# Optimization experiments

Measured on AMD Instinct MI355X. Metric: run time of the kernel, lower is better.

## Reference

```python
import jax, jax.numpy as jnp
import numpy as np

NUM_EXPERTS = 16
TOP_K = 2
INTER = 448  # per-expert intermediate dim


def setup_inputs() -> dict:
    key = jax.random.key(0)
    k1, k2, k3, k4, k5 = jax.random.split(key, 5)
    B, S, H = 4, 2048, 4096
    scale = 0.02
    return {
        "hid": jax.random.normal(k1, (B, S, H), dtype=jnp.float32),
        "gate_w": jax.random.normal(k2, (NUM_EXPERTS, H), dtype=jnp.float32) * scale,
        "u": jax.random.normal(k3, (NUM_EXPERTS * INTER, H), dtype=jnp.float32) * scale,
        "g": jax.random.normal(k4, (NUM_EXPERTS * INTER, H), dtype=jnp.float32) * scale,
        "d": jax.random.normal(k5, (H, NUM_EXPERTS * INTER), dtype=jnp.float32) * scale,
    }


def reference(hid, gate_w, u, g, d):
    B, S, H = hid.shape
    x = hid.reshape(-1, H)  # [bs, H], bs = B*S tokens
    bs = x.shape[0]

    # --- router: softmax over experts, top-k, renormalize, scatter to dense weights ---
    logits = x @ gate_w.T  # [bs, E]
    probs = jax.nn.softmax(logits.astype(jnp.float32), axis=-1)
    vals, idx = jax.lax.top_k(probs, TOP_K)  # [bs, k]
    vals = vals / jnp.sum(vals, axis=-1, keepdims=True)
    rows = jnp.arange(bs)[:, None]
    w = jnp.zeros((bs, NUM_EXPERTS), dtype=jnp.float32).at[rows, idx].set(vals)
    w = w.astype(x.dtype)  # sparse routing weights (zeros off the top-k)

    # --- experts: merged SwiGLU MLP, per-expert 448-wide slices of u/g/d ---
    gate_out = (x @ g.T).reshape(bs, NUM_EXPERTS, INTER)  # [bs, E, I]
    up_out = (x @ u.T).reshape(bs, NUM_EXPERTS, INTER)
    h = jax.nn.silu(gate_out) * up_out  # ir in the original code

    # down proj per expert, weighted by routing weights, summed over experts
    d_r = d.reshape(H, NUM_EXPERTS, INTER)
    out = jnp.einsum("bei,hei,be->bh", h, d_r, w)
    return out.reshape(B, S, H)
```

## Files before the change

### kernel.cpp

```cpp
#include <hip/hip_runtime.h>
#include <hip/hip_bf16.h>
#include <stdint.h>


#define NE    16
#define INTER 448
#define HDIM  4096
#define BS    8192
#define ROWS  (BS * 2)
#define NGU   896
#define CAP   8192

typedef __attribute__((ext_vector_type(8))) _Float16 half8;
typedef __attribute__((ext_vector_type(4))) _Float16 half4;
typedef __attribute__((ext_vector_type(4))) float    f32x4;

__device__ __forceinline__ void gld16(const _Float16* g, _Float16* l) {
    __builtin_amdgcn_global_load_lds(
        (const __attribute__((address_space(1))) void*)g,
        (__attribute__((address_space(3))) void*)l, 16, 0, 0);
}


__global__ __launch_bounds__(256) void k_convert_gu(const float* __restrict__ src,
                                                    _Float16* __restrict__ dst,
                                                    int col_off) {
    int64_t id  = (int64_t)blockIdx.x * 256 + threadIdx.x;
    int64_t k   = (id & 511) * 8;
    int64_t row = id >> 9;
    int     e   = (int)(row / 448);
    int64_t drow = (int64_t)e * NGU + col_off + (row - (int64_t)e * 448);
    const float4* s = reinterpret_cast<const float4*>(src + row * HDIM + k);
    float4 a = s[0], b = s[1];
    half8 o;
    o[0] = (_Float16)a.x; o[1] = (_Float16)a.y; o[2] = (_Float16)a.z; o[3] = (_Float16)a.w;
    o[4] = (_Float16)b.x; o[5] = (_Float16)b.y; o[6] = (_Float16)b.z; o[7] = (_Float16)b.w;
    *reinterpret_cast<half8*>(dst + drow * HDIM + k) = o;
}

__global__ __launch_bounds__(256) void k_convert_flat(const float* __restrict__ src,
                                                      _Float16* __restrict__ dst) {
    int64_t id = ((int64_t)blockIdx.x * 256 + threadIdx.x) * 8;
    const float4* s = reinterpret_cast<const float4*>(src + id);
    float4 a = s[0], b = s[1];
    half8 o;
    o[0] = (_Float16)a.x; o[1] = (_Float16)a.y; o[2] = (_Float16)a.z; o[3] = (_Float16)a.w;
    o[4] = (_Float16)b.x; o[5] = (_Float16)b.y; o[6] = (_Float16)b.z; o[7] = (_Float16)b.w;
    *reinterpret_cast<half8*>(dst + id) = o;
}

__global__ __launch_bounds__(64) void k_router(const float* __restrict__ x,
                                               const float* __restrict__ gw,
                                               _Float16* __restrict__ xh,
                                               int* __restrict__ counts,
                                               int* __restrict__ perm,
                                               float* __restrict__ rw) {
    int t = blockIdx.x;
    int lane = threadIdx.x;
    const float* xr = x + (int64_t)t * HDIM;
    double acc[NE];
#pragma unroll
    for (int e = 0; e < NE; e++) acc[e] = 0.0;
    for (int h = lane * 4; h < HDIM; h += 256) {
        float4 xv = *reinterpret_cast<const float4*>(xr + h);
        half4 o;
        o[0] = (_Float16)xv.x; o[1] = (_Float16)xv.y;
        o[2] = (_Float16)xv.z; o[3] = (_Float16)xv.w;
        *reinterpret_cast<half4*>(xh + (int64_t)t * HDIM + h) = o;
#pragma unroll
        for (int e = 0; e < NE; e++) {
            float4 gv = *reinterpret_cast<const float4*>(gw + e * HDIM + h);
            acc[e] += (double)xv.x * gv.x + (double)xv.y * gv.y
                    + (double)xv.z * gv.z + (double)xv.w * gv.w;
        }
    }
#pragma unroll
    for (int e = 0; e < NE; e++) {
#pragma unroll
        for (int off = 32; off > 0; off >>= 1)
            acc[e] += __shfl_xor(acc[e], off, 64);
    }
    if (lane == 0) {
        int i0 = 0; double l0 = acc[0];
        for (int e = 1; e < NE; e++) if (acc[e] > l0) { l0 = acc[e]; i0 = e; }
        double l1 = -1e300; int i1 = 0;
        for (int e = 0; e < NE; e++) if (e != i0 && acc[e] > l1) { l1 = acc[e]; i1 = e; }
        float w0 = 1.0f / (1.0f + __expf((float)(l1 - l0)));
        float w1 = 1.0f - w0;
        int p0 = atomicAdd(&counts[i0], 1);
        int p1 = atomicAdd(&counts[i1], 1);
        perm[i0 * CAP + p0] = t * 2;
        perm[i1 * CAP + p1] = t * 2 + 1;
        rw[t * 2]     = w0;
        rw[t * 2 + 1] = w1;
    }
}

template <int KTOT, bool DOWN>
__global__ __launch_bounds__(256, 3) void k_gemm(const _Float16* __restrict__ A,
                                                 const _Float16* __restrict__ B,
                                                 const int* __restrict__ counts,
                                                 const int* __restrict__ perm,
                                                 _Float16* __restrict__ gu_out,
                                                 float* __restrict__ out) {
    int e  = blockIdx.z;
    int nt = blockIdx.x;
    int cnt = counts[e];
    __shared__ __align__(16) _Float16 As[128 * 32];
    __shared__ __align__(16) _Float16 Bs[128 * 32];
    __shared__ int perm_s[128];
    int tid  = threadIdx.x;
    int lane = tid & 63, wave = tid >> 6;
    int wm = wave >> 1, wn = wave & 1;
    int lm = lane & 15, lq = lane >> 4;

    int rrow = lane >> 2;
    int cseg = (lane & 3) * 8;
    int row0 = wave * 16 + rrow;
    int row1 = 64 + wave * 16 + rrow;
    _Float16* As0 = &As[(wave * 16) * 32];
    _Float16* As1 = &As[(64 + wave * 16) * 32];
    _Float16* Bs0 = &Bs[(wave * 16) * 32];
    _Float16* Bs1 = &Bs[(64 + wave * 16) * 32];

    const _Float16 *b0, *b1;
    if (DOWN) {
        b0 = B + (int64_t)(nt * 128 + row0) * (NE * INTER) + e * INTER + cseg;
        b1 = B + (int64_t)(nt * 128 + row1) * (NE * INTER) + e * INTER + cseg;
    } else {
        b0 = B + ((int64_t)e * NGU + nt * 128 + row0) * HDIM + cseg;
        b1 = B + ((int64_t)e * NGU + nt * 128 + row1) * HDIM + cseg;
    }

    for (int mt = blockIdx.y; mt * 128 < cnt; mt += gridDim.y) {
        __syncthreads();
        if (tid < 128) {
            int r = mt * 128 + tid;
            perm_s[tid] = (r < cnt) ? perm[e * CAP + r] : -1;
        }
        __syncthreads();
        int pr0 = perm_s[row0], pr1 = perm_s[row1];
        const _Float16 *a0, *a1;
        if (DOWN) {
            a0 = A + (pr0 < 0 ? 0 : (int64_t)pr0 * INTER) + cseg;
            a1 = A + (pr1 < 0 ? 0 : (int64_t)pr1 * INTER) + cseg;
        } else {
            a0 = A + (pr0 < 0 ? 0 : (int64_t)(pr0 >> 1) * HDIM) + cseg;
            a1 = A + (pr1 < 0 ? 0 : (int64_t)(pr1 >> 1) * HDIM) + cseg;
        }
        const _Float16 *bb0 = b0, *bb1 = b1;

        f32x4 acc[4][4];
#pragma unroll
        for (int i = 0; i < 4; i++)
#pragma unroll
            for (int j = 0; j < 4; j++) acc[i][j] = (f32x4){0.f, 0.f, 0.f, 0.f};

#pragma unroll 1
        for (int kt = 0; kt < KTOT; kt += 32) {
            gld16(a0,  As0);  gld16(a1,  As1);
            gld16(bb0, Bs0);  gld16(bb1, Bs1);
            a0 += 32; a1 += 32; bb0 += 32; bb1 += 32;
            __syncthreads();
            half8 af[4], bfr[4];
#pragma unroll
            for (int mi = 0; mi < 4; mi++)
                af[mi] = *reinterpret_cast<const half8*>(&As[(wm * 64 + mi * 16 + lm) * 32 + lq * 8]);
#pragma unroll
            for (int ni = 0; ni < 4; ni++)
                bfr[ni] = *reinterpret_cast<const half8*>(&Bs[(wn * 64 + ni * 16 + lm) * 32 + lq * 8]);
#pragma unroll
            for (int mi = 0; mi < 4; mi++)
#pragma unroll
                for (int ni = 0; ni < 4; ni++)
                    acc[mi][ni] = __builtin_amdgcn_mfma_f32_16x16x32_f16(af[mi], bfr[ni], acc[mi][ni], 0, 0, 0);
            __syncthreads();
        }
#pragma unroll
        for (int mi = 0; mi < 4; mi++) {
#pragma unroll
            for (int r = 0; r < 4; r++) {
                int row = wm * 64 + mi * 16 + lq * 4 + r;
                int g = perm_s[row];
                if (g < 0) continue;
#pragma unroll
                for (int ni = 0; ni < 4; ni++) {
                    int col = nt * 128 + wn * 64 + ni * 16 + lm;
                    float v = acc[mi][ni][r];
                    if (DOWN) atomicAdd(&out[(int64_t)(g >> 1) * HDIM + col], v);
                    else      gu_out[(int64_t)g * NGU + col] = (_Float16)v;
                }
            }
        }
    }
}

__global__ __launch_bounds__(256) void k_swiglu(const _Float16* __restrict__ gu,
                                                const float* __restrict__ rw,
                                                _Float16* __restrict__ h) {
    int64_t id  = (int64_t)blockIdx.x * 256 + threadIdx.x;
    int64_t row = id / 56;
    int64_t j   = (id - row * 56) * 8;
    float w = rw[row];
    half8 gv = *reinterpret_cast<const half8*>(gu + row * NGU + j);
    half8 uv = *reinterpret_cast<const half8*>(gu + row * NGU + 448 + j);
    half8 o;
#pragma unroll
    for (int i = 0; i < 8; i++) {
        float g = (float)gv[i];
        float u = (float)uv[i];
        float s = g / (1.0f + __expf(-g));
        o[i] = (_Float16)(s * u * w);
    }
    *reinterpret_cast<half8*>(h + row * INTER + j) = o;
}

extern "C" void kernel_launch(void* const* d_in, const int* in_sizes, int n_in,
                              void* d_out, int out_size, void* d_ws, size_t ws_size,
                              hipStream_t stream) {
    (void)in_sizes; (void)n_in; (void)ws_size;
    const float* hid    = (const float*)d_in[0];
    const float* gate_w = (const float*)d_in[1];
    const float* u      = (const float*)d_in[2];
    const float* g      = (const float*)d_in[3];
    const float* d      = (const float*)d_in[4];
    float* out = (float*)d_out;

    char* w = (char*)d_ws;
    _Float16* xh    = (_Float16*)(w);
    _Float16* wgu   = (_Float16*)(w + 67108864);
    _Float16* d16   = (_Float16*)(w + 184549376);
    _Float16* gu    = (_Float16*)(w + 243269632);
    _Float16* hbuf  = (_Float16*)(w + 272629760);
    int*      perm  = (int*)     (w + 287309824);
    float*    rw    = (float*)   (w + 287834112);
    int*      cnts  = (int*)     (w + 287899648);

    hipMemsetAsync(d_out, 0, (size_t)out_size * sizeof(float), stream);
    hipMemsetAsync(cnts, 0, 64, stream);

    k_convert_gu<<<14336, 256, 0, stream>>>(g, wgu, 0);
    k_convert_gu<<<14336, 256, 0, stream>>>(u, wgu, 448);
    k_convert_flat<<<14336, 256, 0, stream>>>(d, d16);
    k_router<<<BS, 64, 0, stream>>>(hid, gate_w, xh, cnts, perm, rw);
    k_gemm<HDIM, false><<<dim3(7, 16, NE), 256, 0, stream>>>(xh, wgu, cnts, perm, gu, out);
    k_swiglu<<<3584, 256, 0, stream>>>(gu, rw, hbuf);
    k_gemm<INTER, true><<<dim3(32, 16, NE), 256, 0, stream>>>(hbuf, d16, cnts, perm, gu, out);
}
```

Measured before the change: 1.262 ms.

## Split-K the gate/up expert GEMM with fp32 atomic accumulation

The gate/up grouped GEMM now splits its K dimension (4096) into two halves across the z grid. Partial sums are accumulated with atomicAdd into a zeroed fp32 buffer, and the SwiGLU kernel reads that fp32 buffer. Launch bounds are raised to 6 waves per SIMD. The workspace is compacted so the down-proj fp16 weights reuse the gate/up weight buffer, which means converting d now happens after the first GEMM. The aim is more parallelism and occupancy for the large GEMM, at the cost of an extra 56MB memset, fp32 atomic traffic, and a larger intermediate to read back.

```diff
diff --git a/kernel.cpp b/kernel.cpp
--- a/kernel.cpp
+++ b/kernel.cpp
@@ -96,16 +96,19 @@
     }
 }
 
-template <int KTOT, bool DOWN>
-__global__ __launch_bounds__(256, 3) void k_gemm(const _Float16* __restrict__ A,
+template <int KTOT, int KSPLIT, bool DOWN>
+__global__ __launch_bounds__(256, 6) void k_gemm(const _Float16* __restrict__ A,
                                                  const _Float16* __restrict__ B,
                                                  const int* __restrict__ counts,
                                                  const int* __restrict__ perm,
-                                                 _Float16* __restrict__ gu_out,
+                                                 float* __restrict__ gu32,
                                                  float* __restrict__ out) {
-    int e  = blockIdx.z;
+    int e  = blockIdx.z & (NE - 1);
+    int ks = blockIdx.z >> 4;
     int nt = blockIdx.x;
     int cnt = counts[e];
+    const int KLEN = KTOT / KSPLIT;
+    const int k0   = ks * KLEN;
     __shared__ __align__(16) _Float16 As[128 * 32];
     __shared__ __align__(16) _Float16 Bs[128 * 32];
     __shared__ int perm_s[128];
@@ -125,11 +128,11 @@
 
     const _Float16 *b0, *b1;
     if (DOWN) {
-        b0 = B + (int64_t)(nt * 128 + row0) * (NE * INTER) + e * INTER + cseg;
-        b1 = B + (int64_t)(nt * 128 + row1) * (NE * INTER) + e * INTER + cseg;
+        b0 = B + (int64_t)(nt * 128 + row0) * (NE * INTER) + e * INTER + k0 + cseg;
+        b1 = B + (int64_t)(nt * 128 + row1) * (NE * INTER) + e * INTER + k0 + cseg;
     } else {
-        b0 = B + ((int64_t)e * NGU + nt * 128 + row0) * HDIM + cseg;
-        b1 = B + ((int64_t)e * NGU + nt * 128 + row1) * HDIM + cseg;
+        b0 = B + ((int64_t)e * NGU + nt * 128 + row0) * HDIM + k0 + cseg;
+        b1 = B + ((int64_t)e * NGU + nt * 128 + row1) * HDIM + k0 + cseg;
     }
 
     for (int mt = blockIdx.y; mt * 128 < cnt; mt += gridDim.y) {
@@ -142,11 +145,11 @@
         int pr0 = perm_s[row0], pr1 = perm_s[row1];
         const _Float16 *a0, *a1;
         if (DOWN) {
-            a0 = A + (pr0 < 0 ? 0 : (int64_t)pr0 * INTER) + cseg;
-            a1 = A + (pr1 < 0 ? 0 : (int64_t)pr1 * INTER) + cseg;
+            a0 = A + (pr0 < 0 ? 0 : (int64_t)pr0 * INTER) + k0 + cseg;
+            a1 = A + (pr1 < 0 ? 0 : (int64_t)pr1 * INTER) + k0 + cseg;
         } else {
-            a0 = A + (pr0 < 0 ? 0 : (int64_t)(pr0 >> 1) * HDIM) + cseg;
-            a1 = A + (pr1 < 0 ? 0 : (int64_t)(pr1 >> 1) * HDIM) + cseg;
+            a0 = A + (pr0 < 0 ? 0 : (int64_t)(pr0 >> 1) * HDIM) + k0 + cseg;
+            a1 = A + (pr1 < 0 ? 0 : (int64_t)(pr1 >> 1) * HDIM) + k0 + cseg;
         }
         const _Float16 *bb0 = b0, *bb1 = b1;
 
@@ -157,7 +160,7 @@
             for (int j = 0; j < 4; j++) acc[i][j] = (f32x4){0.f, 0.f, 0.f, 0.f};
 
 #pragma unroll 1
-        for (int kt = 0; kt < KTOT; kt += 32) {
+        for (int kt = 0; kt < KLEN; kt += 32) {
             gld16(a0,  As0);  gld16(a1,  As1);
             gld16(bb0, Bs0);  gld16(bb1, Bs1);
             a0 += 32; a1 += 32; bb0 += 32; bb1 += 32;
@@ -188,29 +191,32 @@
                     int col = nt * 128 + wn * 64 + ni * 16 + lm;
                     float v = acc[mi][ni][r];
                     if (DOWN) atomicAdd(&out[(int64_t)(g >> 1) * HDIM + col], v);
-                    else      gu_out[(int64_t)g * NGU + col] = (_Float16)v;
+                    else      atomicAdd(&gu32[(int64_t)g * NGU + col], v);
                 }
             }
         }
     }
 }
 
-__global__ __launch_bounds__(256) void k_swiglu(const _Float16* __restrict__ gu,
+__global__ __launch_bounds__(256) void k_swiglu(const float* __restrict__ gu,
                                                 const float* __restrict__ rw,
                                                 _Float16* __restrict__ h) {
     int64_t id  = (int64_t)blockIdx.x * 256 + threadIdx.x;
     int64_t row = id / 56;
     int64_t j   = (id - row * 56) * 8;
     float w = rw[row];
-    half8 gv = *reinterpret_cast<const half8*>(gu + row * NGU + j);
-    half8 uv = *reinterpret_cast<const half8*>(gu + row * NGU + 448 + j);
+    float4 g0 = *reinterpret_cast<const float4*>(gu + row * NGU + j);
+    float4 g1 = *reinterpret_cast<const float4*>(gu + row * NGU + j + 4);
+    float4 u0 = *reinterpret_cast<const float4*>(gu + row * NGU + 448 + j);
+    float4 u1 = *reinterpret_cast<const float4*>(gu + row * NGU + 448 + j + 4);
+    float gv[8] = {g0.x, g0.y, g0.z, g0.w, g1.x, g1.y, g1.z, g1.w};
+    float uv[8] = {u0.x, u0.y, u0.z, u0.w, u1.x, u1.y, u1.z, u1.w};
     half8 o;
 #pragma unroll
     for (int i = 0; i < 8; i++) {
-        float g = (float)gv[i];
-        float u = (float)uv[i];
+        float g = gv[i];
         float s = g / (1.0f + __expf(-g));
-        o[i] = (_Float16)(s * u * w);
+        o[i] = (_Float16)(s * uv[i] * w);
     }
     *reinterpret_cast<half8*>(h + row * INTER + j) = o;
 }
@@ -229,21 +235,22 @@
     char* w = (char*)d_ws;
     _Float16* xh    = (_Float16*)(w);
     _Float16* wgu   = (_Float16*)(w + 67108864);
-    _Float16* d16   = (_Float16*)(w + 184549376);
-    _Float16* gu    = (_Float16*)(w + 243269632);
-    _Float16* hbuf  = (_Float16*)(w + 272629760);
-    int*      perm  = (int*)     (w + 287309824);
-    float*    rw    = (float*)   (w + 287834112);
-    int*      cnts  = (int*)     (w + 287899648);
+    _Float16* d16   = (_Float16*)(w + 67108864);
+    float*    gu32  = (float*)   (w + 184549376);
+    _Float16* hbuf  = (_Float16*)(w + 243269632);
+    int*      perm  = (int*)     (w + 257949696);
+    float*    rw    = (float*)   (w + 258473984);
+    int*      cnts  = (int*)     (w + 258539520);
 
     hipMemsetAsync(d_out, 0, (size_t)out_size * sizeof(float), stream);
+    hipMemsetAsync(gu32, 0, 58720256, stream);
     hipMemsetAsync(cnts, 0, 64, stream);
 
     k_convert_gu<<<14336, 256, 0, stream>>>(g, wgu, 0);
     k_convert_gu<<<14336, 256, 0, stream>>>(u, wgu, 448);
+    k_router<<<BS, 64, 0, stream>>>(hid, gate_w, xh, cnts, perm, rw);
+    k_gemm<HDIM, 2, false><<<dim3(7, 16, 32), 256, 0, stream>>>(xh, wgu, cnts, perm, gu32, out);
     k_convert_flat<<<14336, 256, 0, stream>>>(d, d16);
-    k_router<<<BS, 64, 0, stream>>>(hid, gate_w, xh, cnts, perm, rw);
-    k_gemm<HDIM, false><<<dim3(7, 16, NE), 256, 0, stream>>>(xh, wgu, cnts, perm, gu, out);
-    k_swiglu<<<3584, 256, 0, stream>>>(gu, rw, hbuf);
-    k_gemm<INTER, true><<<dim3(32, 16, NE), 256, 0, stream>>>(hbuf, d16, cnts, perm, gu, out);
-}
+    k_swiglu<<<3584, 256, 0, stream>>>(gu32, rw, hbuf);
+    k_gemm<INTER, 1, true><<<dim3(32, 16, NE), 256, 0, stream>>>(hbuf, d16, cnts, perm, gu32, out);
+}
```

Result: slower. 2.652 ms (+110.2%).

## Split down-projection by top-k slot to replace atomics with plain stores

Applied to the files above, without the earlier changes.

The router now also builds a second permutation keyed by (expert, top-k slot). The down-projection runs in two launches: slot 0 writes output rows directly and slot 1 adds to them with a plain read-modify-write. This removes the float atomicAdd traffic and the full output memset, because every token has exactly one entry per slot and so no two blocks touch the same output row within a launch. It also reuses the gate/up weight buffer for the fp16 down weights (convert_flat now runs after the gate/up GEMM) and halves grid.y for the down GEMM. The cost is a second launch and an extra read of the output in pass two.

```diff
diff --git a/kernel.cpp b/kernel.cpp
--- a/kernel.cpp
+++ b/kernel.cpp
@@ -54,6 +54,7 @@
                                                _Float16* __restrict__ xh,
                                                int* __restrict__ counts,
                                                int* __restrict__ perm,
+                                               int* __restrict__ pperm,
                                                float* __restrict__ rw) {
     int t = blockIdx.x;
     int lane = threadIdx.x;
@@ -91,21 +92,28 @@
         int p1 = atomicAdd(&counts[i1], 1);
         perm[i0 * CAP + p0] = t * 2;
         perm[i1 * CAP + p1] = t * 2 + 1;
+        int q0 = atomicAdd(&counts[16 + i0 * 2], 1);
+        int q1 = atomicAdd(&counts[16 + i1 * 2 + 1], 1);
+        pperm[(i0 * 2) * CAP + q0]     = t * 2;
+        pperm[(i1 * 2 + 1) * CAP + q1] = t * 2 + 1;
         rw[t * 2]     = w0;
         rw[t * 2 + 1] = w1;
     }
 }
 
-template <int KTOT, bool DOWN>
+template <int KTOT, bool DOWN, bool ACCUM>
 __global__ __launch_bounds__(256, 3) void k_gemm(const _Float16* __restrict__ A,
                                                  const _Float16* __restrict__ B,
                                                  const int* __restrict__ counts,
                                                  const int* __restrict__ perm,
                                                  _Float16* __restrict__ gu_out,
-                                                 float* __restrict__ out) {
-    int e  = blockIdx.z;
+                                                 float* __restrict__ out,
+                                                 int gsel) {
+    int z  = blockIdx.z;
+    int gi = DOWN ? (z * 2 + gsel) : z;
+    int e  = z;
     int nt = blockIdx.x;
-    int cnt = counts[e];
+    int cnt = counts[gi];
     __shared__ __align__(16) _Float16 As[128 * 32];
     __shared__ __align__(16) _Float16 Bs[128 * 32];
     __shared__ int perm_s[128];
@@ -136,7 +144,7 @@
         __syncthreads();
         if (tid < 128) {
             int r = mt * 128 + tid;
-            perm_s[tid] = (r < cnt) ? perm[e * CAP + r] : -1;
+            perm_s[tid] = (r < cnt) ? perm[gi * CAP + r] : -1;
         }
         __syncthreads();
         int pr0 = perm_s[row0], pr1 = perm_s[row1];
@@ -187,8 +195,13 @@
                 for (int ni = 0; ni < 4; ni++) {
                     int col = nt * 128 + wn * 64 + ni * 16 + lm;
                     float v = acc[mi][ni][r];
-                    if (DOWN) atomicAdd(&out[(int64_t)(g >> 1) * HDIM + col], v);
-                    else      gu_out[(int64_t)g * NGU + col] = (_Float16)v;
+                    if (DOWN) {
+                        int64_t o = (int64_t)(g >> 1) * HDIM + col;
+                        if (ACCUM) out[o] += v;
+                        else       out[o] = v;
+                    } else {
+                        gu_out[(int64_t)g * NGU + col] = (_Float16)v;
+                    }
                 }
             }
         }
@@ -218,7 +231,7 @@
 extern "C" void kernel_launch(void* const* d_in, const int* in_sizes, int n_in,
                               void* d_out, int out_size, void* d_ws, size_t ws_size,
                               hipStream_t stream) {
-    (void)in_sizes; (void)n_in; (void)ws_size;
+    (void)in_sizes; (void)n_in; (void)ws_size; (void)out_size;
     const float* hid    = (const float*)d_in[0];
     const float* gate_w = (const float*)d_in[1];
     const float* u      = (const float*)d_in[2];
@@ -229,21 +242,22 @@
     char* w = (char*)d_ws;
     _Float16* xh    = (_Float16*)(w);
     _Float16* wgu   = (_Float16*)(w + 67108864);
-    _Float16* d16   = (_Float16*)(w + 184549376);
-    _Float16* gu    = (_Float16*)(w + 243269632);
-    _Float16* hbuf  = (_Float16*)(w + 272629760);
-    int*      perm  = (int*)     (w + 287309824);
-    float*    rw    = (float*)   (w + 287834112);
-    int*      cnts  = (int*)     (w + 287899648);
-
-    hipMemsetAsync(d_out, 0, (size_t)out_size * sizeof(float), stream);
-    hipMemsetAsync(cnts, 0, 64, stream);
+    _Float16* d16   = (_Float16*)(w + 67108864);
+    _Float16* gu    = (_Float16*)(w + 184549376);
+    _Float16* hbuf  = (_Float16*)(w + 213909504);
+    int*      perm  = (int*)     (w + 228589568);
+    int*      pperm = (int*)     (w + 229113856);
+    float*    rw    = (float*)   (w + 230162432);
+    int*      cnts  = (int*)     (w + 230227968);
+
+    hipMemsetAsync(cnts, 0, 256, stream);
 
     k_convert_gu<<<14336, 256, 0, stream>>>(g, wgu, 0);
     k_convert_gu<<<14336, 256, 0, stream>>>(u, wgu, 448);
+    k_router<<<BS, 64, 0, stream>>>(hid, gate_w, xh, cnts, perm, pperm, rw);
+    k_gemm<HDIM, false, false><<<dim3(7, 16, NE), 256, 0, stream>>>(xh, wgu, cnts, perm, gu, out, 0);
     k_convert_flat<<<14336, 256, 0, stream>>>(d, d16);
-    k_router<<<BS, 64, 0, stream>>>(hid, gate_w, xh, cnts, perm, rw);
-    k_gemm<HDIM, false><<<dim3(7, 16, NE), 256, 0, stream>>>(xh, wgu, cnts, perm, gu, out);
     k_swiglu<<<3584, 256, 0, stream>>>(gu, rw, hbuf);
-    k_gemm<INTER, true><<<dim3(32, 16, NE), 256, 0, stream>>>(hbuf, d16, cnts, perm, gu, out);
-}
+    k_gemm<INTER, true, false><<<dim3(32, 8, NE), 256, 0, stream>>>(hbuf, d16, cnts + 16, pperm, nullptr, out, 0);
+    k_gemm<INTER, true, true ><<<dim3(32, 8, NE), 256, 0, stream>>>(hbuf, d16, cnts + 16, pperm, nullptr, out, 1);
+}
```

Measured after the change: 1.170 ms. 7.3% less time.
